# Kernel optimization log

Measured on AMD Instinct MI355X. Metric: run time of the kernel, lower is better.

## Reference

```python
import jax, jax.numpy as jnp
import numpy as np

EPS = 1e-12  # matches torch F.normalize default eps

def setup_inputs() -> dict:
    key = jax.random.key(0)
    k1, k2 = jax.random.split(key)
    N, D = 16384, 1024
    pc_feat = jax.random.normal(k1, (N, D), dtype=jnp.float32)
    aug_feat = jax.random.normal(k2, (N, D), dtype=jnp.float32)
    return {"pc_feat": pc_feat, "aug_feat": aug_feat}

def reference(pc_feat, aug_feat):
    # F.normalize(x, dim=1): x / max(||x||_2, eps)
    pc_n = pc_feat / jnp.maximum(jnp.linalg.norm(pc_feat, axis=1, keepdims=True), EPS)
    aug_n = aug_feat / jnp.maximum(jnp.linalg.norm(aug_feat, axis=1, keepdims=True), EPS)
    # diag(pc_n @ aug_n.T) == row-wise dot product; avoids the O(N^2) matmul
    cos = jnp.sum(pc_n * aug_n, axis=1)  # [N]
    # loss = sum(1 - cos) / N == mean(1 - cos)
    return jnp.mean(1.0 - cos)
```

## Files before the change

kernel.cpp:

```cpp
#include <hip/hip_runtime.h>


#define N_ROWS 16384
#define DIM_V4 256
#define TPB 256
#define WAVES_PER_BLOCK (TPB / 64)
#define BLOCKS (N_ROWS / WAVES_PER_BLOCK)

__global__ __launch_bounds__(TPB) void cos_rows_kernel(
    const float4* __restrict__ a, const float4* __restrict__ b,
    float* __restrict__ partial)
{
    const int wave = threadIdx.x >> 6;
    const int lane = threadIdx.x & 63;
    const int r = blockIdx.x * WAVES_PER_BLOCK + wave;

    const float4* ap = a + (size_t)r * DIM_V4;
    const float4* bp = b + (size_t)r * DIM_V4;

    float4 x[4], y[4];
    #pragma unroll
    for (int k = 0; k < 4; ++k) x[k] = ap[lane + 64 * k];
    #pragma unroll
    for (int k = 0; k < 4; ++k) y[k] = bp[lane + 64 * k];

    float ab = 0.0f, aa = 0.0f, bb = 0.0f;
    #pragma unroll
    for (int k = 0; k < 4; ++k) {
        ab += x[k].x * y[k].x + x[k].y * y[k].y + x[k].z * y[k].z + x[k].w * y[k].w;
        aa += x[k].x * x[k].x + x[k].y * x[k].y + x[k].z * x[k].z + x[k].w * x[k].w;
        bb += y[k].x * y[k].x + y[k].y * y[k].y + y[k].z * y[k].z + y[k].w * y[k].w;
    }

    #pragma unroll
    for (int off = 32; off > 0; off >>= 1) {
        ab += __shfl_down(ab, off);
        aa += __shfl_down(aa, off);
        bb += __shfl_down(bb, off);
    }

    __shared__ float s[WAVES_PER_BLOCK];
    if (lane == 0) {
        float na = fmaxf(sqrtf(aa), 1e-12f);
        float nb = fmaxf(sqrtf(bb), 1e-12f);
        s[wave] = ab / (na * nb);
    }
    __syncthreads();
    if (threadIdx.x == 0) {
        float t = 0.0f;
        #pragma unroll
        for (int i = 0; i < WAVES_PER_BLOCK; ++i) t += s[i];
        partial[blockIdx.x] = t;
    }
}

__global__ __launch_bounds__(1024) void finalize_kernel(
    const float* __restrict__ partial, float* __restrict__ out)
{
    const int wave = threadIdx.x >> 6;
    const int lane = threadIdx.x & 63;
    float t = 0.0f;
    #pragma unroll
    for (int i = 0; i < BLOCKS / 1024; ++i) t += partial[threadIdx.x + 1024 * i];
    #pragma unroll
    for (int off = 32; off > 0; off >>= 1) t += __shfl_down(t, off);
    __shared__ float s[1024 / 64];
    if (lane == 0) s[wave] = t;
    __syncthreads();
    if (threadIdx.x == 0) {
        float tot = 0.0f;
        #pragma unroll
        for (int i = 0; i < 1024 / 64; ++i) tot += s[i];
        out[0] = 1.0f - tot / (float)N_ROWS;
    }
}

extern "C" void kernel_launch(void* const* d_in, const int* in_sizes, int n_in,
                              void* d_out, int out_size, void* d_ws, size_t ws_size,
                              hipStream_t stream) {
    const float4* pc  = (const float4*)d_in[0];
    const float4* aug = (const float4*)d_in[1];
    float* partial = (float*)d_ws;
    float* out = (float*)d_out;

    cos_rows_kernel<<<BLOCKS, TPB, 0, stream>>>(pc, aug, partial);
    finalize_kernel<<<1, 1024, 0, stream>>>(partial, out);
}
```

Baseline: 142.0 us.

## Process four rows per wave with double-buffered register loads

Each wavefront now handles four rows, issuing the next row's global loads before reducing the current one so memory latency overlaps with the dot-product and shuffle reductions. The grid shrinks by four and the finalize kernel reads exactly one partial per thread. This raises register pressure and lowers the block count, which may reduce occupancy and available parallelism.

```diff
diff --git a/kernel.cpp b/kernel.cpp
--- a/kernel.cpp
+++ b/kernel.cpp
@@ -5,46 +5,67 @@
 #define DIM_V4 256
 #define TPB 256
 #define WAVES_PER_BLOCK (TPB / 64)
-#define BLOCKS (N_ROWS / WAVES_PER_BLOCK)
+#define ROWS_PER_WAVE 4
+#define ROWS_PER_BLOCK (WAVES_PER_BLOCK * ROWS_PER_WAVE)
+#define BLOCKS (N_ROWS / ROWS_PER_BLOCK)
 
-__global__ __launch_bounds__(TPB) void cos_rows_kernel(
+__global__ __launch_bounds__(TPB, 4) void cos_rows_kernel(
     const float4* __restrict__ a, const float4* __restrict__ b,
     float* __restrict__ partial)
 {
     const int wave = threadIdx.x >> 6;
     const int lane = threadIdx.x & 63;
-    const int r = blockIdx.x * WAVES_PER_BLOCK + wave;
+    const int gw = blockIdx.x * WAVES_PER_BLOCK + wave;
+    const size_t base = (size_t)gw * ROWS_PER_WAVE * DIM_V4 + lane;
+    const float4* ap = a + base;
+    const float4* bp = b + base;
 
-    const float4* ap = a + (size_t)r * DIM_V4;
-    const float4* bp = b + (size_t)r * DIM_V4;
+    float4 xa[4], ya[4], xb[4], yb[4];
+    float wsum = 0.0f;
 
-    float4 x[4], y[4];
-    #pragma unroll
-    for (int k = 0; k < 4; ++k) x[k] = ap[lane + 64 * k];
-    #pragma unroll
-    for (int k = 0; k < 4; ++k) y[k] = bp[lane + 64 * k];
+#define LOAD_ROW(X, Y, RI) do {                                         \
+    const float4* _ar = ap + (RI) * DIM_V4;                             \
+    const float4* _br = bp + (RI) * DIM_V4;                             \
+    _Pragma("unroll") for (int k = 0; k < 4; ++k) X[k] = _ar[64 * k];   \
+    _Pragma("unroll") for (int k = 0; k < 4; ++k) Y[k] = _br[64 * k];   \
+} while (0)
 
-    float ab = 0.0f, aa = 0.0f, bb = 0.0f;
-    #pragma unroll
-    for (int k = 0; k < 4; ++k) {
-        ab += x[k].x * y[k].x + x[k].y * y[k].y + x[k].z * y[k].z + x[k].w * y[k].w;
-        aa += x[k].x * x[k].x + x[k].y * x[k].y + x[k].z * x[k].z + x[k].w * x[k].w;
-        bb += y[k].x * y[k].x + y[k].y * y[k].y + y[k].z * y[k].z + y[k].w * y[k].w;
-    }
+#define DOT_ROW(X, Y) do {                                              \
+    float ab = 0.f, aa = 0.f, bb = 0.f;                                 \
+    _Pragma("unroll") for (int k = 0; k < 4; ++k) {                     \
+        ab += X[k].x * Y[k].x + X[k].y * Y[k].y                         \
+            + X[k].z * Y[k].z + X[k].w * Y[k].w;                        \
+        aa += X[k].x * X[k].x + X[k].y * X[k].y                         \
+            + X[k].z * X[k].z + X[k].w * X[k].w;                        \
+        bb += Y[k].x * Y[k].x + Y[k].y * Y[k].y                         \
+            + Y[k].z * Y[k].z + Y[k].w * Y[k].w;                        \
+    }                                                                   \
+    _Pragma("unroll") for (int off = 32; off > 0; off >>= 1) {          \
+        ab += __shfl_down(ab, off);                                     \
+        aa += __shfl_down(aa, off);                                     \
+        bb += __shfl_down(bb, off);                                     \
+    }                                                                   \
+    if (lane == 0) {                                                    \
+        float na = fmaxf(sqrtf(aa), 1e-12f);                            \
+        float nb = fmaxf(sqrtf(bb), 1e-12f);                            \
+        wsum += ab / (na * nb);                                         \
+    }                                                                   \
+} while (0)
 
-    #pragma unroll
-    for (int off = 32; off > 0; off >>= 1) {
-        ab += __shfl_down(ab, off);
-        aa += __shfl_down(aa, off);
-        bb += __shfl_down(bb, off);
-    }
+    LOAD_ROW(xa, ya, 0);
+    LOAD_ROW(xb, yb, 1);
+    DOT_ROW(xa, ya);
+    LOAD_ROW(xa, ya, 2);
+    DOT_ROW(xb, yb);
+    LOAD_ROW(xb, yb, 3);
+    DOT_ROW(xa, ya);
+    DOT_ROW(xb, yb);
+
+#undef LOAD_ROW
+#undef DOT_ROW
 
     __shared__ float s[WAVES_PER_BLOCK];
-    if (lane == 0) {
-        float na = fmaxf(sqrtf(aa), 1e-12f);
-        float nb = fmaxf(sqrtf(bb), 1e-12f);
-        s[wave] = ab / (na * nb);
-    }
+    if (lane == 0) s[wave] = wsum;
     __syncthreads();
     if (threadIdx.x == 0) {
         float t = 0.0f;
@@ -59,9 +80,7 @@
 {
     const int wave = threadIdx.x >> 6;
     const int lane = threadIdx.x & 63;
-    float t = 0.0f;
-    #pragma unroll
-    for (int i = 0; i < BLOCKS / 1024; ++i) t += partial[threadIdx.x + 1024 * i];
+    float t = partial[threadIdx.x];
     #pragma unroll
     for (int off = 32; off > 0; off >>= 1) t += __shfl_down(t, off);
     __shared__ float s[1024 / 64];
```

New measurement: 146.2 us. +3.0%, slower.

## Process four rows per wave with software-pipelined double-buffered loads

Applied to the files above, without the earlier changes.

Each wave now handles four rows instead of one. Loads for the next rows are issued before the current rows' dot products are computed, with sched barriers to keep that order, so more memory requests are in flight per wave. The shuffle reductions for two rows are batched together, and the block count drops fourfold, which shrinks the finalize kernel's input to one element per thread. The cost is higher register pressure (launch bounds with 4 blocks per SM) and fewer blocks, which could reduce occupancy-driven latency hiding.

```diff
diff --git a/kernel.cpp b/kernel.cpp
--- a/kernel.cpp
+++ b/kernel.cpp
@@ -4,52 +4,91 @@
 #define N_ROWS 16384
 #define DIM_V4 256
 #define TPB 256
-#define WAVES_PER_BLOCK (TPB / 64)
-#define BLOCKS (N_ROWS / WAVES_PER_BLOCK)
+#define WPB (TPB / 64)
+#define RPW 4
+#define BLOCKS (N_ROWS / (WPB * RPW))
 
-__global__ __launch_bounds__(TPB) void cos_rows_kernel(
-    const float4* __restrict__ a, const float4* __restrict__ b,
-    float* __restrict__ partial)
-{
-    const int wave = threadIdx.x >> 6;
-    const int lane = threadIdx.x & 63;
-    const int r = blockIdx.x * WAVES_PER_BLOCK + wave;
+__device__ __forceinline__ void load_row(const float4* __restrict__ p, float4 v[4]) {
+    #pragma unroll
+    for (int k = 0; k < 4; ++k) v[k] = p[64 * k];
+}
 
-    const float4* ap = a + (size_t)r * DIM_V4;
-    const float4* bp = b + (size_t)r * DIM_V4;
-
-    float4 x[4], y[4];
-    #pragma unroll
-    for (int k = 0; k < 4; ++k) x[k] = ap[lane + 64 * k];
-    #pragma unroll
-    for (int k = 0; k < 4; ++k) y[k] = bp[lane + 64 * k];
-
-    float ab = 0.0f, aa = 0.0f, bb = 0.0f;
+__device__ __forceinline__ void dot_row(const float4 x[4], const float4 y[4],
+                                        float& ab, float& aa, float& bb) {
+    ab = 0.f; aa = 0.f; bb = 0.f;
     #pragma unroll
     for (int k = 0; k < 4; ++k) {
         ab += x[k].x * y[k].x + x[k].y * y[k].y + x[k].z * y[k].z + x[k].w * y[k].w;
         aa += x[k].x * x[k].x + x[k].y * x[k].y + x[k].z * x[k].z + x[k].w * x[k].w;
         bb += y[k].x * y[k].x + y[k].y * y[k].y + y[k].z * y[k].z + y[k].w * y[k].w;
     }
+}
 
+__device__ __forceinline__ void reduce2_accum(int lane,
+        float ab0, float aa0, float bb0,
+        float ab1, float aa1, float bb1, float& wsum) {
     #pragma unroll
     for (int off = 32; off > 0; off >>= 1) {
-        ab += __shfl_down(ab, off);
-        aa += __shfl_down(aa, off);
-        bb += __shfl_down(bb, off);
+        ab0 += __shfl_down(ab0, off);
+        aa0 += __shfl_down(aa0, off);
+        bb0 += __shfl_down(bb0, off);
+        ab1 += __shfl_down(ab1, off);
+        aa1 += __shfl_down(aa1, off);
+        bb1 += __shfl_down(bb1, off);
     }
+    if (lane == 0) {
+        float na0 = fmaxf(sqrtf(aa0), 1e-12f);
+        float nb0 = fmaxf(sqrtf(bb0), 1e-12f);
+        float na1 = fmaxf(sqrtf(aa1), 1e-12f);
+        float nb1 = fmaxf(sqrtf(bb1), 1e-12f);
+        wsum += ab0 / (na0 * nb0) + ab1 / (na1 * nb1);
+    }
+}
 
-    __shared__ float s[WAVES_PER_BLOCK];
-    if (lane == 0) {
-        float na = fmaxf(sqrtf(aa), 1e-12f);
-        float nb = fmaxf(sqrtf(bb), 1e-12f);
-        s[wave] = ab / (na * nb);
-    }
+__global__ __launch_bounds__(TPB, 4) void cos_rows_kernel(
+    const float4* __restrict__ a, const float4* __restrict__ b,
+    float* __restrict__ partial)
+{
+    const int wave = threadIdx.x >> 6;
+    const int lane = threadIdx.x & 63;
+    const int gw = blockIdx.x * WPB + wave;
+    const size_t base = (size_t)gw * RPW * DIM_V4 + lane;
+    const float4* ap = a + base;
+    const float4* bp = b + base;
+
+    float4 x0[4], y0[4], x1[4], y1[4];
+    float ab0, aa0, bb0, ab1, aa1, bb1;
+    float wsum = 0.0f;
+
+    load_row(ap + 0 * DIM_V4, x0);
+    load_row(bp + 0 * DIM_V4, y0);
+    load_row(ap + 1 * DIM_V4, x1);
+    load_row(bp + 1 * DIM_V4, y1);
+    __builtin_amdgcn_sched_barrier(0);
+
+    dot_row(x0, y0, ab0, aa0, bb0);
+    load_row(ap + 2 * DIM_V4, x0);
+    load_row(bp + 2 * DIM_V4, y0);
+    __builtin_amdgcn_sched_barrier(0);
+
+    dot_row(x1, y1, ab1, aa1, bb1);
+    load_row(ap + 3 * DIM_V4, x1);
+    load_row(bp + 3 * DIM_V4, y1);
+    __builtin_amdgcn_sched_barrier(0);
+
+    reduce2_accum(lane, ab0, aa0, bb0, ab1, aa1, bb1, wsum);
+
+    dot_row(x0, y0, ab0, aa0, bb0);
+    dot_row(x1, y1, ab1, aa1, bb1);
+    reduce2_accum(lane, ab0, aa0, bb0, ab1, aa1, bb1, wsum);
+
+    __shared__ float s[WPB];
+    if (lane == 0) s[wave] = wsum;
     __syncthreads();
     if (threadIdx.x == 0) {
         float t = 0.0f;
         #pragma unroll
-        for (int i = 0; i < WAVES_PER_BLOCK; ++i) t += s[i];
+        for (int i = 0; i < WPB; ++i) t += s[i];
         partial[blockIdx.x] = t;
     }
 }
@@ -59,9 +98,7 @@
 {
     const int wave = threadIdx.x >> 6;
     const int lane = threadIdx.x & 63;
-    float t = 0.0f;
-    #pragma unroll
-    for (int i = 0; i < BLOCKS / 1024; ++i) t += partial[threadIdx.x + 1024 * i];
+    float t = partial[threadIdx.x];
     #pragma unroll
     for (int off = 32; off > 0; off >>= 1) t += __shfl_down(t, off);
     __shared__ float s[1024 / 64];
```

Result: slower. 144.9 us (+2.1%).

## Process eight rows per block with block-wide row striding

Applied to the files above, without the earlier changes.

Reassigns work so each 256-thread block handles 8 rows, with every thread loading one float4 per row from both inputs, instead of one wave per row. Per-row partial sums are reduced by wave shuffles and then across waves through shared memory before the normalization. The aim is more loads in flight per thread and fewer blocks, at the cost of many more shuffle reductions and an extra shared-memory stage. The finalize kernel is specialized to the reduced block count.

```diff
diff --git a/kernel.cpp b/kernel.cpp
--- a/kernel.cpp
+++ b/kernel.cpp
@@ -4,53 +4,75 @@
 #define N_ROWS 16384
 #define DIM_V4 256
 #define TPB 256
-#define WAVES_PER_BLOCK (TPB / 64)
-#define BLOCKS (N_ROWS / WAVES_PER_BLOCK)
+#define RPB 8
+#define BLOCKS (N_ROWS / RPB)
 
-__global__ __launch_bounds__(TPB) void cos_rows_kernel(
+__global__ __launch_bounds__(TPB, 8) void cos_rows_kernel(
     const float4* __restrict__ a, const float4* __restrict__ b,
     float* __restrict__ partial)
 {
-    const int wave = threadIdx.x >> 6;
-    const int lane = threadIdx.x & 63;
-    const int r = blockIdx.x * WAVES_PER_BLOCK + wave;
+    const int t = threadIdx.x;
+    const int wave = t >> 6;
+    const int lane = t & 63;
+    const size_t base = (size_t)blockIdx.x * RPB * DIM_V4 + t;
+    const float4* ap = a + base;
+    const float4* bp = b + base;
 
-    const float4* ap = a + (size_t)r * DIM_V4;
-    const float4* bp = b + (size_t)r * DIM_V4;
+    float ab[RPB], aa[RPB], bb[RPB];
 
-    float4 x[4], y[4];
     #pragma unroll
-    for (int k = 0; k < 4; ++k) x[k] = ap[lane + 64 * k];
-    #pragma unroll
-    for (int k = 0; k < 4; ++k) y[k] = bp[lane + 64 * k];
-
-    float ab = 0.0f, aa = 0.0f, bb = 0.0f;
-    #pragma unroll
-    for (int k = 0; k < 4; ++k) {
-        ab += x[k].x * y[k].x + x[k].y * y[k].y + x[k].z * y[k].z + x[k].w * y[k].w;
-        aa += x[k].x * x[k].x + x[k].y * x[k].y + x[k].z * x[k].z + x[k].w * x[k].w;
-        bb += y[k].x * y[k].x + y[k].y * y[k].y + y[k].z * y[k].z + y[k].w * y[k].w;
+    for (int r = 0; r < RPB; r += 2) {
+        float4 x0 = ap[(r + 0) * DIM_V4];
+        float4 y0 = bp[(r + 0) * DIM_V4];
+        float4 x1 = ap[(r + 1) * DIM_V4];
+        float4 y1 = bp[(r + 1) * DIM_V4];
+        ab[r]     = x0.x*y0.x + x0.y*y0.y + x0.z*y0.z + x0.w*y0.w;
+        aa[r]     = x0.x*x0.x + x0.y*x0.y + x0.z*x0.z + x0.w*x0.w;
+        bb[r]     = y0.x*y0.x + y0.y*y0.y + y0.z*y0.z + y0.w*y0.w;
+        ab[r + 1] = x1.x*y1.x + x1.y*y1.y + x1.z*y1.z + x1.w*y1.w;
+        aa[r + 1] = x1.x*x1.x + x1.y*x1.y + x1.z*x1.z + x1.w*x1.w;
+        bb[r + 1] = y1.x*y1.x + y1.y*y1.y + y1.z*y1.z + y1.w*y1.w;
     }
 
     #pragma unroll
     for (int off = 32; off > 0; off >>= 1) {
-        ab += __shfl_down(ab, off);
-        aa += __shfl_down(aa, off);
-        bb += __shfl_down(bb, off);
+        #pragma unroll
+        for (int r = 0; r < RPB; ++r) {
+            ab[r] += __shfl_down(ab[r], off);
+            aa[r] += __shfl_down(aa[r], off);
+            bb[r] += __shfl_down(bb[r], off);
+        }
     }
 
-    __shared__ float s[WAVES_PER_BLOCK];
+    __shared__ float s[4][3 * RPB];
+    __shared__ float srow[RPB];
     if (lane == 0) {
-        float na = fmaxf(sqrtf(aa), 1e-12f);
-        float nb = fmaxf(sqrtf(bb), 1e-12f);
-        s[wave] = ab / (na * nb);
+        #pragma unroll
+        for (int r = 0; r < RPB; ++r) {
+            s[wave][3 * r + 0] = ab[r];
+            s[wave][3 * r + 1] = aa[r];
+            s[wave][3 * r + 2] = bb[r];
+        }
     }
     __syncthreads();
-    if (threadIdx.x == 0) {
-        float t = 0.0f;
+    if (t < RPB) {
+        float A = 0.f, B = 0.f, C = 0.f;
         #pragma unroll
-        for (int i = 0; i < WAVES_PER_BLOCK; ++i) t += s[i];
-        partial[blockIdx.x] = t;
+        for (int w = 0; w < 4; ++w) {
+            A += s[w][3 * t + 0];
+            B += s[w][3 * t + 1];
+            C += s[w][3 * t + 2];
+        }
+        float na = fmaxf(sqrtf(B), 1e-12f);
+        float nb = fmaxf(sqrtf(C), 1e-12f);
+        srow[t] = A / (na * nb);
+    }
+    __syncthreads();
+    if (t == 0) {
+        float tot = 0.f;
+        #pragma unroll
+        for (int r = 0; r < RPB; ++r) tot += srow[r];
+        partial[blockIdx.x] = tot;
     }
 }
 
@@ -59,9 +81,7 @@
 {
     const int wave = threadIdx.x >> 6;
     const int lane = threadIdx.x & 63;
-    float t = 0.0f;
-    #pragma unroll
-    for (int i = 0; i < BLOCKS / 1024; ++i) t += partial[threadIdx.x + 1024 * i];
+    float t = partial[threadIdx.x] + partial[threadIdx.x + 1024];
     #pragma unroll
     for (int off = 32; off > 0; off >>= 1) t += __shfl_down(t, off);
     __shared__ float s[1024 / 64];
```

Measured after the change: 145.1 us. +2.2%, slower.
